# Optimization experiments

Measured on AMD Instinct MI355X. Metric: run time of the kernel, lower is better.

## Reference

```python
import jax, jax.numpy as jnp
import numpy as np

BSZ, L, D, K = 4, 4096, 512, 4


def setup_inputs() -> dict:
    key = jax.random.key(0)
    ks = jax.random.split(key, 8)
    n = jnp.arange(D, dtype=jnp.float32)
    f = jnp.sqrt(2.0 * n + 1.0)
    f = f / f.max()
    omega = jnp.exp(-f * np.float32(np.log(10000.0)))  # hippo_freqs(D)
    # freqs are strictly decreasing in n -> argsort descending == arange
    band_idx = jnp.argsort(-omega).reshape(K, D // K).astype(jnp.int32)
    B_vec = jnp.sqrt(2.0 * n + 1.0)
    B_vec = B_vec / B_vec.max()  # hippo_b_vector(D)
    return {
        "x": jax.random.normal(ks[0], (BSZ, L, D), dtype=jnp.float32),
        "z_prev": jax.random.normal(ks[1], (BSZ, L, D), dtype=jnp.float32),
        "W_psi": jax.random.normal(ks[2], (2 * D, D), dtype=jnp.float32) * 0.02,
        "b_psi": jnp.zeros((2 * D,), jnp.float32),
        "W_phi": jax.random.normal(ks[3], (2 * D, D), dtype=jnp.float32) * 0.02,
        "b_phi": jnp.zeros((2 * D,), jnp.float32),
        "W_gate": jax.random.normal(ks[4], (1, D), dtype=jnp.float32) * 0.02,
        "b_gate": jnp.zeros((1,), jnp.float32),
        "omega": omega,
        "log_gamma": jax.random.normal(ks[5], (D,), dtype=jnp.float32) - 3.0,
        "dt": jnp.array(0.1, jnp.float32),
        "surprise_gain": jnp.zeros((1,), jnp.float32),
        "tau": jnp.ones((1,), jnp.float32),
        "beta": jnp.zeros((1,), jnp.float32),
        "B_vec": B_vec,
        "band_idx": band_idx,
    }


def _exact_projection(z):
    # geodesic projection to zero-mean unit-std along last axis
    m = z.mean(-1, keepdims=True)
    v = ((z - m) ** 2).mean(-1, keepdims=True)
    return (z - m) / (jnp.sqrt(v) + 1e-6)


def reference(x, z_prev, W_psi, b_psi, W_phi, b_phi, W_gate, b_gate,
              omega, log_gamma, dt, surprise_gain, tau, beta, B_vec, band_idx):
    B_, L_, D_ = x.shape
    K_ = band_idx.shape[0]

    psi_raw = x @ W_psi.T + b_psi          # [B,L,2D]
    psi = jax.lax.complex(psi_raw[..., :D_], psi_raw[..., D_:])
    phi_raw = x @ W_phi.T + b_phi
    phi = jax.lax.complex(phi_raw[..., :D_], phi_raw[..., D_:])

    gate = jax.nn.sigmoid(x @ W_gate.T + b_gate)          # [B,L,1]
    surprise = jnp.abs(x - z_prev).mean(-1, keepdims=True)
    gate = gate * (1.0 + jnp.tanh(surprise_gain) * surprise)

    U = (gate * B_vec).astype(jnp.complex64) * psi        # [B,L,D] complex

    dta = jnp.abs(dt)
    lam = jax.lax.complex(-jnp.exp(log_gamma), omega)     # [D]
    t = jnp.arange(L_, dtype=jnp.float32)
    kernel = jnp.exp(lam[None, :] * (t[:, None] * dta))   # [L,D] complex, A^t

    n_fft = 2 * L_
    K_freq = jnp.fft.fft(kernel.T, n=n_fft, axis=1)                 # [D,2L]
    U_freq = jnp.fft.fft(jnp.transpose(U, (0, 2, 1)), n=n_fft, axis=2)  # [B,D,2L]
    H = jnp.fft.ifft(U_freq * K_freq[None], axis=2)[:, :, :L_]
    H = jnp.transpose(H, (0, 2, 1))                        # [B,L,D] complex

    H_proj = jax.lax.complex(_exact_projection(H.real), _exact_projection(H.imag))

    Hb = H_proj[:, :, band_idx]   # [B,L,K,band]
    Pb = phi[:, :, band_idx]
    alpha = (jnp.conj(Hb) * Pb).sum(-1, keepdims=True) / (D_ // K_)  # [B,L,K,1]
    c_k = jax.nn.softmax(jnp.abs(alpha) / jnp.clip(tau, 1e-4, None), axis=2)
    alpha_ig = alpha * c_k * K_
    density = (Hb.real ** 2 + Hb.imag ** 2).mean(-1, keepdims=True)
    alpha_fin = alpha_ig + (beta * density).astype(alpha_ig.dtype)
    out_bands = (Hb * alpha_fin).real                      # [B,L,K,band]

    out = jnp.zeros((B_, L_, D_), x.dtype).at[:, :, band_idx].set(out_bands)
    return out
```

## Files before the change

kernel.cpp:

```cpp
#include <hip/hip_runtime.h>
#include <hip/hip_bf16.h>
#include <math.h>

#define BSZ   4
#define LSEQ  4096
#define DDIM  512
#define KBAND 4
#define MROWS (BSZ*LSEQ)
#define BLD   (MROWS*DDIM)
#define CHUNK 16
#define NCH   (LSEQ/CHUNK)
#define NGRP  16
#define TBL   ((CHUNK+1)*DDIM)
#define NCOLS 2048

#define FRONT_CVT_BLOCKS  (MROWS/4)
#define FRONT_B_BLOCKS    ((NCOLS*64)/256)
#define FRONT_PREP_BLOCKS ((2*TBL+255)/256)

typedef __attribute__((ext_vector_type(8))) short  short8;
typedef __attribute__((ext_vector_type(8))) unsigned short u16x8;
typedef __attribute__((ext_vector_type(4))) unsigned short u16x4;
typedef __attribute__((ext_vector_type(4))) float  f32x4;

__device__ __forceinline__ unsigned short f2bf(float f) {
    unsigned int u = __float_as_uint(f);
    u = (u + 0x7FFFu + ((u >> 16) & 1u)) >> 16;
    return (unsigned short)u;
}
__device__ __forceinline__ float bf2f(unsigned short h) {
    return __uint_as_float(((unsigned int)h) << 16);
}

__device__ __forceinline__ void gld_lds16(const void* g, void* l) {
    __builtin_amdgcn_global_load_lds(
        (const __attribute__((address_space(1))) void*)g,
        (__attribute__((address_space(3))) void*)l, 16, 0, 0);
}

__global__ void k_front(const float* __restrict__ x,
                        const float* __restrict__ z_prev,
                        const float* __restrict__ Wg,
                        const float* __restrict__ bg,
                        const float* __restrict__ sg,
                        const float* __restrict__ Wpsi,
                        const float* __restrict__ Wphi,
                        const float* __restrict__ omega,
                        const float* __restrict__ log_gamma,
                        const float* __restrict__ dt,
                        const int*   __restrict__ band_idx,
                        float* __restrict__ gate,
                        unsigned short* __restrict__ Ahi,
                        unsigned short* __restrict__ Alo,
                        unsigned short* __restrict__ Bhi,
                        unsigned short* __restrict__ Blo,
                        float* __restrict__ apR, float* __restrict__ apI,
                        float* __restrict__ apgR, float* __restrict__ apgI,
                        int* __restrict__ bandOf, int* __restrict__ posOf)
{
    int bid = blockIdx.x;
    int tid = threadIdx.x;

    if (bid < FRONT_CVT_BLOCKS) {
        int m    = bid * 4 + (tid >> 6);
        int lane = tid & 63;
        const float4* xr = (const float4*)(x      + ((size_t)m << 9));
        const float4* zr = (const float4*)(z_prev + ((size_t)m << 9));
        const float4* wg = (const float4*)Wg;
        float dot = 0.f, sur = 0.f;
        int msw = m & 7;
#pragma unroll
        for (int i = 0; i < 2; i++) {
            int e = lane + i*64;
            float4 a = xr[e];
            float4 z = zr[e];
            float4 w = wg[e];
            dot += a.x*w.x + a.y*w.y + a.z*w.z + a.w*w.w;
            sur += fabsf(a.x-z.x) + fabsf(a.y-z.y) + fabsf(a.z-z.z) + fabsf(a.w-z.w);
            float fa[4] = {a.x, a.y, a.z, a.w};
            u16x4 h, l;
#pragma unroll
            for (int j = 0; j < 4; ++j) {
                unsigned short hb = f2bf(fa[j]);
                h[j] = hb;
                l[j] = f2bf(fa[j] - bf2f(hb));
            }
            int grp = e >> 1, half = e & 1;
            int chunk = grp >> 3, gs = grp & 7;
            int gd = gs ^ msw;
            size_t dst = ((size_t)m << 9) + chunk*64 + gd*8 + half*4;
            *(u16x4*)(Ahi + dst) = h;
            *(u16x4*)(Alo + dst) = l;
        }
#pragma unroll
        for (int mm = 32; mm; mm >>= 1) { dot += __shfl_xor(dot, mm); sur += __shfl_xor(sur, mm); }
        if (lane == 0) {
            float g = 1.f / (1.f + expf(-(dot + bg[0])));
            g *= (1.f + tanhf(sg[0]) * (sur * (1.f/512.f)));
            gate[m] = g;
        }
    } else if (bid < FRONT_CVT_BLOCKS + FRONT_B_BLOCKS) {
        int gid = (bid - FRONT_CVT_BLOCKS) * 256 + tid;
        int n = gid >> 6, grp = gid & 63;
        int chunk = grp >> 3, g = grp & 7;
        int se = chunk*64 + ((g ^ (n & 7)) << 3);
        const float* wp = (n < 1024) ? (Wpsi + ((size_t)n << 9) + se)
                                     : (Wphi + ((size_t)(n - 1024) << 9) + se);
        u16x8 h, l;
#pragma unroll
        for (int j = 0; j < 8; ++j) {
            float f = wp[j];
            unsigned short hb = f2bf(f);
            h[j] = hb;
            l[j] = f2bf(f - bf2f(hb));
        }
        size_t dst = ((size_t)n << 9) + grp*8;
        *(u16x8*)(Bhi + dst) = h;
        *(u16x8*)(Blo + dst) = l;
    } else {
        int gid = (bid - FRONT_CVT_BLOCKS - FRONT_B_BLOCKS) * 256 + tid;
        float dta = fabsf(dt[0]);
        if (gid < TBL) {
            int k = gid / DDIM, d = gid % DDIM;
            float g = -expf(log_gamma[d]);
            float w = omega[d];
            float e = expf(g * dta * (float)k);
            float s, c;
            sincosf(w * dta * (float)k, &s, &c);
            apR[gid] = e * c;
            apI[gid] = e * s;
        } else if (gid < 2*TBL) {
            int gg = gid - TBL;
            int k = gg / DDIM, d = gg % DDIM;
            float g = -expf(log_gamma[d]);
            float w = omega[d];
            float ph = dta * (float)(16 * k);
            float e = expf(g * ph);
            float s, c;
            sincosf(w * ph, &s, &c);
            apgR[gg] = e * c;
            apgI[gg] = e * s;
        }
        if (gid < DDIM) {
            int d = band_idx[gid];
            bandOf[d] = gid >> 7;
            posOf[d]  = gid & 127;
        }
    }
}

__global__ __launch_bounds__(256)
void k_gemm_bf16(const unsigned short* __restrict__ Ahi,
                 const unsigned short* __restrict__ Alo,
                 const unsigned short* __restrict__ Bhi,
                 const unsigned short* __restrict__ Blo,
                 const float* __restrict__ bpsi, const float* __restrict__ bphi,
                 float* __restrict__ psiR, float* __restrict__ psiI,
                 float* __restrict__ phiR, float* __restrict__ phiI)
{
    __shared__ __align__(16) char As[16384];
    __shared__ __align__(16) char Bs[16384];

    int bid = blockIdx.x;
    int wg  = (bid & 7) * 256 + (bid >> 3);
    int m0 = (wg >> 4) * 128;
    int n0 = (wg & 15) * 128;

    int tid  = threadIdx.x;
    int lane = tid & 63;
    int wv   = tid >> 6;
    int wm = wv >> 1, wn = wv & 1;
    int lr = lane & 15, lk = lane >> 4;

    f32x4 acc[4][4];
#pragma unroll
    for (int mi = 0; mi < 4; ++mi)
#pragma unroll
        for (int ni = 0; ni < 4; ++ni) acc[mi][ni] = (f32x4)0.f;

    for (int s = 0; s < 24; ++s) {
        const unsigned short* Asrc = (s >= 8 && s < 16) ? Alo : Ahi;
        const unsigned short* Bsrc = (s < 16) ? Bhi : Blo;
        int kb2 = (s & 7) << 7;

        __syncthreads();
#pragma unroll
        for (int i = 0; i < 4; ++i) {
            int flat = tid + i * 256;
            int r = flat >> 3, g = flat & 7;
            size_t goff = ((size_t)r << 10) + kb2 + g * 16;
            gld_lds16((const char*)Asrc + ((size_t)m0 << 10) + goff,
                      As + (wv * 64 + i * 256) * 16);
            gld_lds16((const char*)Bsrc + ((size_t)n0 << 10) + goff,
                      Bs + (wv * 64 + i * 256) * 16);
        }
        __syncthreads();

#pragma unroll
        for (int kk = 0; kk < 2; ++kk) {
            int tb = (kk * 64 + lk * 16) ^ ((lr & 7) << 4);
            short8 af[4], bfr[4];
#pragma unroll
            for (int mi = 0; mi < 4; ++mi) {
                int r = wm * 64 + mi * 16 + lr;
                af[mi] = *(const short8*)(As + r * 128 + tb);
            }
#pragma unroll
            for (int ni = 0; ni < 4; ++ni) {
                int r = wn * 64 + ni * 16 + lr;
                bfr[ni] = *(const short8*)(Bs + r * 128 + tb);
            }
#pragma unroll
            for (int mi = 0; mi < 4; ++mi)
#pragma unroll
                for (int ni = 0; ni < 4; ++ni)
                    acc[mi][ni] = __builtin_amdgcn_mfma_f32_16x16x32_bf16(
                        af[mi], bfr[ni], acc[mi][ni], 0, 0, 0);
        }
    }

#pragma unroll
    for (int ni = 0; ni < 4; ++ni) {
        int ncol = n0 + wn * 64 + ni * 16 + lr;
        float bias = (ncol < 1024) ? bpsi[ncol] : bphi[ncol - 1024];
        int p = ncol >> 9;
        float* plane = (p == 0) ? psiR : (p == 1) ? psiI : (p == 2) ? phiR : phiI;
        int col = ncol & 511;
#pragma unroll
        for (int mi = 0; mi < 4; ++mi) {
            int mrow = m0 + wm * 64 + mi * 16 + lk * 4;
#pragma unroll
            for (int j = 0; j < 4; ++j)
                plane[(size_t)(mrow + j) * 512 + col] = acc[mi][ni][j] + bias;
        }
    }
}

__launch_bounds__(512)
__global__ void k_scanc(const float* __restrict__ UR, const float* __restrict__ UI,
                        const float* __restrict__ gate,
                        const float* __restrict__ Bvec,
                        const float* __restrict__ apR, const float* __restrict__ apI,
                        float* __restrict__ carR, float* __restrict__ carI)
{
    int b = blockIdx.x >> 8;
    int c = blockIdx.x & 255;
    int d = threadIdx.x;
    float ar = apR[DDIM + d], ai = apI[DDIM + d];
    float bv = Bvec[d];
    int t0 = c * CHUNK;
    size_t base = ((size_t)b * LSEQ + t0) * DDIM + d;
    const float* grow = gate + (size_t)b * LSEQ + t0;

    float ur[CHUNK], ui[CHUNK];
#pragma unroll
    for (int t = 0; t < CHUNK; t++) {
        ur[t] = UR[base + (size_t)t * DDIM];
        ui[t] = UI[base + (size_t)t * DDIM];
    }
    float hr = 0.f, hi = 0.f;
#pragma unroll
    for (int t = 0; t < CHUNK; t++) {
        float g  = grow[t] * bv;
        float nr = ar*hr - ai*hi + g * ur[t];
        float ni = ar*hi + ai*hr + g * ui[t];
        hr = nr; hi = ni;
    }
    size_t ci = ((size_t)(b * NCH + c)) * DDIM + d;
    carR[ci] = hr; carI[ci] = hi;
}

__launch_bounds__(512)
__global__ void k_carry(float* __restrict__ carR, float* __restrict__ carI,
                        const float* __restrict__ apR, const float* __restrict__ apI,
                        const float* __restrict__ apgR, const float* __restrict__ apgI)
{
    __shared__ float totR[NGRP][32], totI[NGRP][32];
    __shared__ float excR[NGRP][32], excI[NGRP][32];

    int b    = blockIdx.x >> 4;
    int dblk = blockIdx.x & 15;
    int tid  = threadIdx.x;
    int cg   = tid >> 5;
    int dl   = tid & 31;
    int d    = dblk * 32 + dl;

    float qr = apR[CHUNK*DDIM + d], qi = apI[CHUNK*DDIM + d];
    size_t i0 = ((size_t)(b * NCH + cg * 16)) * DDIM + d;

    float pr[16], pi[16];
#pragma unroll
    for (int j = 0; j < 16; j++) {
        pr[j] = carR[i0 + (size_t)j * DDIM];
        pi[j] = carI[i0 + (size_t)j * DDIM];
    }
#pragma unroll
    for (int j = 1; j < 16; j++) {
        float nr = qr*pr[j-1] - qi*pi[j-1] + pr[j];
        float ni = qr*pi[j-1] + qi*pr[j-1] + pi[j];
        pr[j] = nr; pi[j] = ni;
    }
    totR[cg][dl] = pr[15];
    totI[cg][dl] = pi[15];
    __syncthreads();

    if (tid < 32) {
        int dd = dblk * 32 + tid;
        float Qr = apgR[16*DDIM + dd], Qi = apgI[16*DDIM + dd];
        float Pr = 0.f, Pi = 0.f;
#pragma unroll
        for (int g = 0; g < NGRP; g++) {
            excR[g][tid] = Pr; excI[g][tid] = Pi;
            float nr = Qr*Pr - Qi*Pi + totR[g][tid];
            float ni = Qr*Pi + Qi*Pr + totI[g][tid];
            Pr = nr; Pi = ni;
        }
    }
    __syncthreads();

    float Er = excR[cg][dl], Ei = excI[cg][dl];
    bool hasE = (cg > 0);
#pragma unroll
    for (int j = 0; j < 16; j++) {
        float rr = pr[j], ii = pi[j];
        if (hasE) {
            float fr = apgR[(j+1)*DDIM + d], fi = apgI[(j+1)*DDIM + d];
            rr += fr*Er - fi*Ei;
            ii += fr*Ei + fi*Er;
        }
        carR[i0 + (size_t)j * DDIM] = rr;
        carI[i0 + (size_t)j * DDIM] = ii;
    }
}

__launch_bounds__(512)
__global__ void k_out(const float* __restrict__ UR, const float* __restrict__ UI,
                      const float* __restrict__ phR, const float* __restrict__ phI,
                      const float* __restrict__ carR, const float* __restrict__ carI,
                      const float* __restrict__ apR, const float* __restrict__ apI,
                      const float* __restrict__ gate, const float* __restrict__ Bvec,
                      const float* __restrict__ tau, const float* __restrict__ beta,
                      float* __restrict__ out)
{
    __shared__ float p1[2][8][16];
    __shared__ float p2[2][8][16];

    int row0 = blockIdx.x * CHUNK;
    int b = row0 >> 12;
    int c = (row0 & 4095) >> 4;
    int d = threadIdx.x;
    int w = d >> 6, lane = d & 63;
    int kb = d >> 7;

    float ar = apR[DDIM + d], ai_ = apI[DDIM + d];
    float bv = Bvec[d];
    const float* grow = gate + row0;

    float cr = 0.f, cm = 0.f;
    bool hasCar = (c > 0);
    if (hasCar) {
        size_t ci = ((size_t)(b * NCH + (c - 1))) * DDIM + d;
        cr = carR[ci]; cm = carI[ci];
    }

    float tv = tau[0]; tv = (tv < 1e-4f) ? 1e-4f : tv;
    float bt_s = beta[0];

    float sr = 0.f, si_ = 0.f;

    for (int wnd = 0; wnd < 4; ++wnd) {
        int pb = wnd & 1;

        float hr[4], hi[4], ppr[4], ppi[4];
#pragma unroll
        for (int r = 0; r < 4; ++r) {
            int rowt = wnd*4 + r;
            size_t idx = ((size_t)(row0 + rowt) << 9) + d;
            ppr[r] = phR[idx]; ppi[r] = phI[idx];
            float g = grow[rowt] * bv;
            float nr = ar*sr - ai_*si_ + g * UR[idx];
            float ni = ar*si_ + ai_*sr + g * UI[idx];
            sr = nr; si_ = ni;
            hr[r] = sr; hi[r] = si_;
            if (hasCar) {
                float apr = apR[(rowt+1)*DDIM + d], api = apI[(rowt+1)*DDIM + d];
                hr[r] += apr*cr - api*cm;
                hi[r] += apr*cm + api*cr;
            }
        }

        float s0[4], s1[4], s2[4], s3[4];
#pragma unroll
        for (int r = 0; r < 4; ++r) {
            s0[r] = hr[r]; s1[r] = hi[r];
            s2[r] = hr[r]*hr[r]; s3[r] = hi[r]*hi[r];
        }
#pragma unroll
        for (int m = 32; m; m >>= 1) {
#pragma unroll
            for (int r = 0; r < 4; ++r) {
                s0[r] += __shfl_xor(s0[r], m); s1[r] += __shfl_xor(s1[r], m);
                s2[r] += __shfl_xor(s2[r], m); s3[r] += __shfl_xor(s3[r], m);
            }
        }
        if (lane == 0) {
#pragma unroll
            for (int r = 0; r < 4; ++r) {
                p1[pb][w][r*4+0] = s0[r]; p1[pb][w][r*4+1] = s1[r];
                p1[pb][w][r*4+2] = s2[r]; p1[pb][w][r*4+3] = s3[r];
            }
        }
        __syncthreads();

        float aR[4], aI[4], dn[4];
#pragma unroll
        for (int r = 0; r < 4; ++r) {
            float Sr = 0.f, Si = 0.f, Sr2 = 0.f, Si2 = 0.f;
#pragma unroll
            for (int ww = 0; ww < 8; ++ww) {
                Sr  += p1[pb][ww][r*4+0]; Si  += p1[pb][ww][r*4+1];
                Sr2 += p1[pb][ww][r*4+2]; Si2 += p1[pb][ww][r*4+3];
            }
            float mr = Sr * (1.f/512.f), mi = Si * (1.f/512.f);
            float vr = Sr2 * (1.f/512.f) - mr*mr;
            float vi = Si2 * (1.f/512.f) - mi*mi;
            float Hpr = (hr[r] - mr) / (sqrtf(vr) + 1e-6f);
            float Hpi = (hi[r] - mi) / (sqrtf(vi) + 1e-6f);
            hr[r] = Hpr; hi[r] = Hpi;
            aR[r] = Hpr*ppr[r] + Hpi*ppi[r];
            aI[r] = Hpr*ppi[r] - Hpi*ppr[r];
            dn[r] = Hpr*Hpr + Hpi*Hpi;
        }

#pragma unroll
        for (int m = 32; m; m >>= 1) {
#pragma unroll
            for (int r = 0; r < 4; ++r) {
                aR[r] += __shfl_xor(aR[r], m);
                aI[r] += __shfl_xor(aI[r], m);
                dn[r] += __shfl_xor(dn[r], m);
            }
        }
        if (lane == 0) {
#pragma unroll
            for (int r = 0; r < 4; ++r) {
                p2[pb][w][r*4+0] = aR[r]; p2[pb][w][r*4+1] = aI[r];
                p2[pb][w][r*4+2] = dn[r];
            }
        }
        __syncthreads();

#pragma unroll
        for (int r = 0; r < 4; ++r) {
            float aRk[4], aIk[4], dnk[4], mag[4];
            float mx = -1e30f;
#pragma unroll
            for (int k = 0; k < 4; k++) {
                aRk[k] = (p2[pb][2*k][r*4+0] + p2[pb][2*k+1][r*4+0]) * (1.f/128.f);
                aIk[k] = (p2[pb][2*k][r*4+1] + p2[pb][2*k+1][r*4+1]) * (1.f/128.f);
                dnk[k] = (p2[pb][2*k][r*4+2] + p2[pb][2*k+1][r*4+2]) * (1.f/128.f);
                mag[k] = sqrtf(aRk[k]*aRk[k] + aIk[k]*aIk[k]) / tv;
                mx = fmaxf(mx, mag[k]);
            }
            float se = 0.f, ek[4];
#pragma unroll
            for (int k = 0; k < 4; k++) { ek[k] = expf(mag[k] - mx); se += ek[k]; }
            float inv = 1.f / se;
            float ck  = ek[kb] * inv;
            float afR = aRk[kb] * ck * 4.f + bt_s * dnk[kb];
            float afI = aIk[kb] * ck * 4.f;
            size_t idx = ((size_t)(row0 + wnd*4 + r) << 9) + d;
            out[idx] = hr[r] * afR - hi[r] * afI;
        }
    }
}

extern "C" void kernel_launch(void* const* d_in, const int* in_sizes, int n_in,
                              void* d_out, int out_size, void* d_ws, size_t ws_size,
                              hipStream_t stream)
{
    const float* x        = (const float*)d_in[0];
    const float* z_prev   = (const float*)d_in[1];
    const float* W_psi    = (const float*)d_in[2];
    const float* b_psi    = (const float*)d_in[3];
    const float* W_phi    = (const float*)d_in[4];
    const float* b_phi    = (const float*)d_in[5];
    const float* W_gate   = (const float*)d_in[6];
    const float* b_gate   = (const float*)d_in[7];
    const float* omega    = (const float*)d_in[8];
    const float* log_gam  = (const float*)d_in[9];
    const float* dt       = (const float*)d_in[10];
    const float* sg       = (const float*)d_in[11];
    const float* tau      = (const float*)d_in[12];
    const float* beta     = (const float*)d_in[13];
    const float* B_vec    = (const float*)d_in[14];
    const int*   band_idx = (const int*)d_in[15];
    float* out = (float*)d_out;
    float* ws  = (float*)d_ws;

    float* psiR = ws;
    float* psiI = psiR + BLD;
    float* phiR = psiI + BLD;
    float* phiI = phiR + BLD;
    float* gate = phiI + BLD;
    float* apR  = gate + MROWS;
    float* apI  = apR + TBL;
    float* apgR = apI + TBL;
    float* apgI = apgR + TBL;
    float* carR = apgI + TBL;
    float* carI = carR + (size_t)BSZ*NCH*DDIM;
    int* bandOf = (int*)(carI + (size_t)BSZ*NCH*DDIM);
    int* posOf  = bandOf + DDIM;
    unsigned short* Bhi = (unsigned short*)(posOf + DDIM);
    unsigned short* Blo = Bhi + (size_t)NCOLS*512;

    unsigned short* Ahi = (unsigned short*)d_out;
    unsigned short* Alo = Ahi + (size_t)MROWS*512;

    k_front<<<FRONT_CVT_BLOCKS + FRONT_B_BLOCKS + FRONT_PREP_BLOCKS, 256, 0, stream>>>(
        x, z_prev, W_gate, b_gate, sg, W_psi, W_phi, omega, log_gam, dt, band_idx,
        gate, Ahi, Alo, Bhi, Blo, apR, apI, apgR, apgI, bandOf, posOf);

    k_gemm_bf16<<<(MROWS/128) * (NCOLS/128), 256, 0, stream>>>(
        Ahi, Alo, Bhi, Blo, b_psi, b_phi, psiR, psiI, phiR, phiI);

    k_scanc<<<BSZ * NCH, 512, 0, stream>>>(psiR, psiI, gate, B_vec, apR, apI, carR, carI);

    k_carry<<<BSZ * 16, 512, 0, stream>>>(carR, carI, apR, apI, apgR, apgI);

    k_out<<<MROWS/CHUNK, 512, 0, stream>>>(psiR, psiI, phiR, phiI, carR, carI,
                                           apR, apI, gate, B_vec, tau, beta, out);
}
```

Before: 407.1 us.

## Shrink scan chunk to four rows and vectorize scan/output kernels per thread

Reduces the chunked linear-recurrence chunk size from 16 to 4 timesteps and restructures the scan-carry and output kernels. Each thread now handles four contiguous channels with float4 loads, and each block handles four chunks. The carry kernel is rebalanced to 32 groups of 32 chunks. The output kernel drops its sequential four-window loop with double-buffered reductions in favour of a single pass with fewer syncs. The aim is more parallelism, wider memory accesses and a shorter serial dependency chain, at the cost of a larger carry array and a deeper carry-propagation pass.

```diff
diff --git a/kernel.cpp b/kernel.cpp
--- a/kernel.cpp
+++ b/kernel.cpp
@@ -5,18 +5,19 @@
 #define BSZ   4
 #define LSEQ  4096
 #define DDIM  512
-#define KBAND 4
 #define MROWS (BSZ*LSEQ)
 #define BLD   (MROWS*DDIM)
-#define CHUNK 16
+#define CHUNK 4
 #define NCH   (LSEQ/CHUNK)
-#define NGRP  16
-#define TBL   ((CHUNK+1)*DDIM)
+#define NCHG  (MROWS/CHUNK)
+#define NGRP  32
+#define TBLA  ((CHUNK+1)*DDIM)
+#define TBLG  (33*DDIM)
 #define NCOLS 2048
 
 #define FRONT_CVT_BLOCKS  (MROWS/4)
 #define FRONT_B_BLOCKS    ((NCOLS*64)/256)
-#define FRONT_PREP_BLOCKS ((2*TBL+255)/256)
+#define FRONT_PREP_BLOCKS ((TBLA+TBLG+255)/256)
 
 typedef __attribute__((ext_vector_type(8))) short  short8;
 typedef __attribute__((ext_vector_type(8))) unsigned short u16x8;
@@ -48,15 +49,13 @@
                         const float* __restrict__ omega,
                         const float* __restrict__ log_gamma,
                         const float* __restrict__ dt,
-                        const int*   __restrict__ band_idx,
                         float* __restrict__ gate,
                         unsigned short* __restrict__ Ahi,
                         unsigned short* __restrict__ Alo,
                         unsigned short* __restrict__ Bhi,
                         unsigned short* __restrict__ Blo,
                         float* __restrict__ apR, float* __restrict__ apI,
-                        float* __restrict__ apgR, float* __restrict__ apgI,
-                        int* __restrict__ bandOf, int* __restrict__ posOf)
+                        float* __restrict__ apgR, float* __restrict__ apgI)
 {
     int bid = blockIdx.x;
     int tid = threadIdx.x;
@@ -120,31 +119,27 @@
     } else {
         int gid = (bid - FRONT_CVT_BLOCKS - FRONT_B_BLOCKS) * 256 + tid;
         float dta = fabsf(dt[0]);
-        if (gid < TBL) {
+        if (gid < TBLA) {
             int k = gid / DDIM, d = gid % DDIM;
             float g = -expf(log_gamma[d]);
             float w = omega[d];
-            float e = expf(g * dta * (float)k);
+            float ph = dta * (float)k;
+            float e = expf(g * ph);
             float s, c;
-            sincosf(w * dta * (float)k, &s, &c);
+            sincosf(w * ph, &s, &c);
             apR[gid] = e * c;
             apI[gid] = e * s;
-        } else if (gid < 2*TBL) {
-            int gg = gid - TBL;
+        } else if (gid < TBLA + TBLG) {
+            int gg = gid - TBLA;
             int k = gg / DDIM, d = gg % DDIM;
             float g = -expf(log_gamma[d]);
             float w = omega[d];
-            float ph = dta * (float)(16 * k);
+            float ph = dta * (float)(4 * k);
             float e = expf(g * ph);
             float s, c;
             sincosf(w * ph, &s, &c);
             apgR[gg] = e * c;
             apgI[gg] = e * s;
-        }
-        if (gid < DDIM) {
-            int d = band_idx[gid];
-            bandOf[d] = gid >> 7;
-            posOf[d]  = gid & 127;
         }
     }
 }
@@ -243,31 +238,35 @@
                         const float* __restrict__ apR, const float* __restrict__ apI,
                         float* __restrict__ carR, float* __restrict__ carI)
 {
-    int b = blockIdx.x >> 8;
-    int c = blockIdx.x & 255;
-    int d = threadIdx.x;
-    float ar = apR[DDIM + d], ai = apI[DDIM + d];
-    float bv = Bvec[d];
-    int t0 = c * CHUNK;
-    size_t base = ((size_t)b * LSEQ + t0) * DDIM + d;
-    const float* grow = gate + (size_t)b * LSEQ + t0;
-
-    float ur[CHUNK], ui[CHUNK];
-#pragma unroll
-    for (int t = 0; t < CHUNK; t++) {
-        ur[t] = UR[base + (size_t)t * DDIM];
-        ui[t] = UI[base + (size_t)t * DDIM];
-    }
-    float hr = 0.f, hi = 0.f;
-#pragma unroll
-    for (int t = 0; t < CHUNK; t++) {
-        float g  = grow[t] * bv;
-        float nr = ar*hr - ai*hi + g * ur[t];
-        float ni = ar*hi + ai*hr + g * ui[t];
-        hr = nr; hi = ni;
-    }
-    size_t ci = ((size_t)(b * NCH + c)) * DDIM + d;
-    carR[ci] = hr; carI[ci] = hi;
+    int tid = threadIdx.x;
+    int g   = tid >> 7;
+    int t   = tid & 127;
+    int cc  = blockIdx.x * 4 + g;
+    int row0 = cc << 2;
+    int dbase = t << 2;
+
+    f32x4 ar = *(const f32x4*)(apR + DDIM + dbase);
+    f32x4 ai = *(const f32x4*)(apI + DDIM + dbase);
+    f32x4 bv = *(const f32x4*)(Bvec + dbase);
+
+    f32x4 sr = (f32x4)0.f, si = (f32x4)0.f;
+#pragma unroll
+    for (int r = 0; r < 4; ++r) {
+        size_t idx = ((size_t)(row0 + r) << 9) + dbase;
+        f32x4 uR = *(const f32x4*)(UR + idx);
+        f32x4 uI = *(const f32x4*)(UI + idx);
+        float gg = gate[row0 + r];
+#pragma unroll
+        for (int j = 0; j < 4; ++j) {
+            float gj = gg * bv[j];
+            float nr = ar[j]*sr[j] - ai[j]*si[j] + gj*uR[j];
+            float ni = ar[j]*si[j] + ai[j]*sr[j] + gj*uI[j];
+            sr[j] = nr; si[j] = ni;
+        }
+    }
+    size_t ci = ((size_t)cc << 9) + dbase;
+    *(f32x4*)(carR + ci) = sr;
+    *(f32x4*)(carI + ci) = si;
 }
 
 __launch_bounds__(512)
@@ -275,38 +274,38 @@
                         const float* __restrict__ apR, const float* __restrict__ apI,
                         const float* __restrict__ apgR, const float* __restrict__ apgI)
 {
-    __shared__ float totR[NGRP][32], totI[NGRP][32];
-    __shared__ float excR[NGRP][32], excI[NGRP][32];
-
-    int b    = blockIdx.x >> 4;
-    int dblk = blockIdx.x & 15;
+    __shared__ float totR[NGRP][16], totI[NGRP][16];
+    __shared__ float excR[NGRP][16], excI[NGRP][16];
+
+    int b    = blockIdx.x >> 5;
+    int dblk = blockIdx.x & 31;
     int tid  = threadIdx.x;
-    int cg   = tid >> 5;
-    int dl   = tid & 31;
-    int d    = dblk * 32 + dl;
+    int cg   = tid >> 4;
+    int dl   = tid & 15;
+    int d    = dblk * 16 + dl;
 
     float qr = apR[CHUNK*DDIM + d], qi = apI[CHUNK*DDIM + d];
-    size_t i0 = ((size_t)(b * NCH + cg * 16)) * DDIM + d;
-
-    float pr[16], pi[16];
-#pragma unroll
-    for (int j = 0; j < 16; j++) {
+    size_t i0 = ((size_t)(b * NCH + cg * 32)) * DDIM + d;
+
+    float pr[32], pi[32];
+#pragma unroll
+    for (int j = 0; j < 32; j++) {
         pr[j] = carR[i0 + (size_t)j * DDIM];
         pi[j] = carI[i0 + (size_t)j * DDIM];
     }
 #pragma unroll
-    for (int j = 1; j < 16; j++) {
+    for (int j = 1; j < 32; j++) {
         float nr = qr*pr[j-1] - qi*pi[j-1] + pr[j];
         float ni = qr*pi[j-1] + qi*pr[j-1] + pi[j];
         pr[j] = nr; pi[j] = ni;
     }
-    totR[cg][dl] = pr[15];
-    totI[cg][dl] = pi[15];
+    totR[cg][dl] = pr[31];
+    totI[cg][dl] = pi[31];
     __syncthreads();
 
-    if (tid < 32) {
-        int dd = dblk * 32 + tid;
-        float Qr = apgR[16*DDIM + dd], Qi = apgI[16*DDIM + dd];
+    if (tid < 16) {
+        int dd = dblk * 16 + tid;
+        float Qr = apgR[32*DDIM + dd], Qi = apgI[32*DDIM + dd];
         float Pr = 0.f, Pi = 0.f;
 #pragma unroll
         for (int g = 0; g < NGRP; g++) {
@@ -319,17 +318,11 @@
     __syncthreads();
 
     float Er = excR[cg][dl], Ei = excI[cg][dl];
-    bool hasE = (cg > 0);
-#pragma unroll
-    for (int j = 0; j < 16; j++) {
-        float rr = pr[j], ii = pi[j];
-        if (hasE) {
-            float fr = apgR[(j+1)*DDIM + d], fi = apgI[(j+1)*DDIM + d];
-            rr += fr*Er - fi*Ei;
-            ii += fr*Ei + fi*Er;
-        }
-        carR[i0 + (size_t)j * DDIM] = rr;
-        carI[i0 + (size_t)j * DDIM] = ii;
+#pragma unroll
+    for (int j = 0; j < 32; j++) {
+        float fr = apgR[(j+1)*DDIM + d], fi = apgI[(j+1)*DDIM + d];
+        carR[i0 + (size_t)j * DDIM] = pr[j] + fr*Er - fi*Ei;
+        carI[i0 + (size_t)j * DDIM] = pi[j] + fr*Ei + fi*Er;
     }
 }
 
@@ -342,136 +335,137 @@
                       const float* __restrict__ tau, const float* __restrict__ beta,
                       float* __restrict__ out)
 {
-    __shared__ float p1[2][8][16];
-    __shared__ float p2[2][8][16];
-
-    int row0 = blockIdx.x * CHUNK;
-    int b = row0 >> 12;
-    int c = (row0 & 4095) >> 4;
-    int d = threadIdx.x;
-    int w = d >> 6, lane = d & 63;
-    int kb = d >> 7;
-
-    float ar = apR[DDIM + d], ai_ = apI[DDIM + d];
-    float bv = Bvec[d];
-    const float* grow = gate + row0;
-
-    float cr = 0.f, cm = 0.f;
-    bool hasCar = (c > 0);
-    if (hasCar) {
-        size_t ci = ((size_t)(b * NCH + (c - 1))) * DDIM + d;
-        cr = carR[ci]; cm = carI[ci];
-    }
-
+    __shared__ float p1[4][2][16];
+    __shared__ float p2[4][4][12];
+
+    int tid  = threadIdx.x;
+    int g    = tid >> 7;
+    int t    = tid & 127;
+    int wv   = (tid >> 6) & 1;
+    int lane = tid & 63;
+    int cc   = blockIdx.x * 4 + g;
+    int ccb  = cc & (NCH - 1);
+    int row0 = cc << 2;
+    int dbase = t << 2;
+    int kb   = t >> 5;
+
+    f32x4 ar = *(const f32x4*)(apR + DDIM + dbase);
+    f32x4 ai = *(const f32x4*)(apI + DDIM + dbase);
+    f32x4 bv = *(const f32x4*)(Bvec + dbase);
+
+    f32x4 cr = (f32x4)0.f, cm = (f32x4)0.f;
+    if (ccb > 0) {
+        size_t ci = ((size_t)(cc - 1) << 9) + dbase;
+        cr = *(const f32x4*)(carR + ci);
+        cm = *(const f32x4*)(carI + ci);
+    }
     float tv = tau[0]; tv = (tv < 1e-4f) ? 1e-4f : tv;
     float bt_s = beta[0];
 
-    float sr = 0.f, si_ = 0.f;
-
-    for (int wnd = 0; wnd < 4; ++wnd) {
-        int pb = wnd & 1;
-
-        float hr[4], hi[4], ppr[4], ppi[4];
+    f32x4 hr[4], hi[4];
+    {
+        f32x4 sr = (f32x4)0.f, si = (f32x4)0.f;
 #pragma unroll
         for (int r = 0; r < 4; ++r) {
-            int rowt = wnd*4 + r;
-            size_t idx = ((size_t)(row0 + rowt) << 9) + d;
-            ppr[r] = phR[idx]; ppi[r] = phI[idx];
-            float g = grow[rowt] * bv;
-            float nr = ar*sr - ai_*si_ + g * UR[idx];
-            float ni = ar*si_ + ai_*sr + g * UI[idx];
-            sr = nr; si_ = ni;
-            hr[r] = sr; hi[r] = si_;
-            if (hasCar) {
-                float apr = apR[(rowt+1)*DDIM + d], api = apI[(rowt+1)*DDIM + d];
-                hr[r] += apr*cr - api*cm;
-                hi[r] += apr*cm + api*cr;
+            size_t idx = ((size_t)(row0 + r) << 9) + dbase;
+            f32x4 uR = *(const f32x4*)(UR + idx);
+            f32x4 uI = *(const f32x4*)(UI + idx);
+            float gg = gate[row0 + r];
+            f32x4 fr = *(const f32x4*)(apR + (r+1)*DDIM + dbase);
+            f32x4 fi = *(const f32x4*)(apI + (r+1)*DDIM + dbase);
+#pragma unroll
+            for (int j = 0; j < 4; ++j) {
+                float gj = gg * bv[j];
+                float nr = ar[j]*sr[j] - ai[j]*si[j] + gj*uR[j];
+                float ni = ar[j]*si[j] + ai[j]*sr[j] + gj*uI[j];
+                sr[j] = nr; si[j] = ni;
+                hr[r][j] = nr + fr[j]*cr[j] - fi[j]*cm[j];
+                hi[r][j] = ni + fr[j]*cm[j] + fi[j]*cr[j];
             }
         }
-
-        float s0[4], s1[4], s2[4], s3[4];
-#pragma unroll
-        for (int r = 0; r < 4; ++r) {
-            s0[r] = hr[r]; s1[r] = hi[r];
-            s2[r] = hr[r]*hr[r]; s3[r] = hi[r]*hi[r];
-        }
-#pragma unroll
-        for (int m = 32; m; m >>= 1) {
-#pragma unroll
-            for (int r = 0; r < 4; ++r) {
-                s0[r] += __shfl_xor(s0[r], m); s1[r] += __shfl_xor(s1[r], m);
-                s2[r] += __shfl_xor(s2[r], m); s3[r] += __shfl_xor(s3[r], m);
-            }
-        }
-        if (lane == 0) {
-#pragma unroll
-            for (int r = 0; r < 4; ++r) {
-                p1[pb][w][r*4+0] = s0[r]; p1[pb][w][r*4+1] = s1[r];
-                p1[pb][w][r*4+2] = s2[r]; p1[pb][w][r*4+3] = s3[r];
-            }
-        }
-        __syncthreads();
-
-        float aR[4], aI[4], dn[4];
-#pragma unroll
-        for (int r = 0; r < 4; ++r) {
-            float Sr = 0.f, Si = 0.f, Sr2 = 0.f, Si2 = 0.f;
-#pragma unroll
-            for (int ww = 0; ww < 8; ++ww) {
-                Sr  += p1[pb][ww][r*4+0]; Si  += p1[pb][ww][r*4+1];
-                Sr2 += p1[pb][ww][r*4+2]; Si2 += p1[pb][ww][r*4+3];
-            }
-            float mr = Sr * (1.f/512.f), mi = Si * (1.f/512.f);
-            float vr = Sr2 * (1.f/512.f) - mr*mr;
-            float vi = Si2 * (1.f/512.f) - mi*mi;
-            float Hpr = (hr[r] - mr) / (sqrtf(vr) + 1e-6f);
-            float Hpi = (hi[r] - mi) / (sqrtf(vi) + 1e-6f);
-            hr[r] = Hpr; hi[r] = Hpi;
-            aR[r] = Hpr*ppr[r] + Hpi*ppi[r];
-            aI[r] = Hpr*ppi[r] - Hpi*ppr[r];
-            dn[r] = Hpr*Hpr + Hpi*Hpi;
-        }
-
-#pragma unroll
-        for (int m = 32; m; m >>= 1) {
-#pragma unroll
-            for (int r = 0; r < 4; ++r) {
-                aR[r] += __shfl_xor(aR[r], m);
-                aI[r] += __shfl_xor(aI[r], m);
-                dn[r] += __shfl_xor(dn[r], m);
-            }
-        }
-        if (lane == 0) {
-#pragma unroll
-            for (int r = 0; r < 4; ++r) {
-                p2[pb][w][r*4+0] = aR[r]; p2[pb][w][r*4+1] = aI[r];
-                p2[pb][w][r*4+2] = dn[r];
-            }
-        }
-        __syncthreads();
-
-#pragma unroll
-        for (int r = 0; r < 4; ++r) {
-            float aRk[4], aIk[4], dnk[4], mag[4];
-            float mx = -1e30f;
-#pragma unroll
-            for (int k = 0; k < 4; k++) {
-                aRk[k] = (p2[pb][2*k][r*4+0] + p2[pb][2*k+1][r*4+0]) * (1.f/128.f);
-                aIk[k] = (p2[pb][2*k][r*4+1] + p2[pb][2*k+1][r*4+1]) * (1.f/128.f);
-                dnk[k] = (p2[pb][2*k][r*4+2] + p2[pb][2*k+1][r*4+2]) * (1.f/128.f);
-                mag[k] = sqrtf(aRk[k]*aRk[k] + aIk[k]*aIk[k]) / tv;
-                mx = fmaxf(mx, mag[k]);
-            }
-            float se = 0.f, ek[4];
-#pragma unroll
-            for (int k = 0; k < 4; k++) { ek[k] = expf(mag[k] - mx); se += ek[k]; }
-            float inv = 1.f / se;
-            float ck  = ek[kb] * inv;
-            float afR = aRk[kb] * ck * 4.f + bt_s * dnk[kb];
-            float afI = aIk[kb] * ck * 4.f;
-            size_t idx = ((size_t)(row0 + wnd*4 + r) << 9) + d;
-            out[idx] = hr[r] * afR - hi[r] * afI;
-        }
+    }
+
+    float s[16];
+#pragma unroll
+    for (int r = 0; r < 4; ++r) {
+        float a0=0.f, a1=0.f, a2=0.f, a3=0.f;
+#pragma unroll
+        for (int j = 0; j < 4; ++j) {
+            a0 += hr[r][j]; a1 += hi[r][j];
+            a2 += hr[r][j]*hr[r][j]; a3 += hi[r][j]*hi[r][j];
+        }
+        s[r*4+0]=a0; s[r*4+1]=a1; s[r*4+2]=a2; s[r*4+3]=a3;
+    }
+#pragma unroll
+    for (int m = 32; m; m >>= 1)
+#pragma unroll
+        for (int v = 0; v < 16; ++v) s[v] += __shfl_xor(s[v], m);
+    if (lane == 0)
+#pragma unroll
+        for (int v = 0; v < 16; ++v) p1[g][wv][v] = s[v];
+    __syncthreads();
+
+    float q[12];
+#pragma unroll
+    for (int r = 0; r < 4; ++r) {
+        float Sr  = p1[g][0][r*4+0] + p1[g][1][r*4+0];
+        float Si  = p1[g][0][r*4+1] + p1[g][1][r*4+1];
+        float Sr2 = p1[g][0][r*4+2] + p1[g][1][r*4+2];
+        float Si2 = p1[g][0][r*4+3] + p1[g][1][r*4+3];
+        float mr = Sr * (1.f/512.f), mi = Si * (1.f/512.f);
+        float vr = Sr2 * (1.f/512.f) - mr*mr;
+        float vi = Si2 * (1.f/512.f) - mi*mi;
+        float rvr = 1.f / (sqrtf(vr) + 1e-6f);
+        float rvi = 1.f / (sqrtf(vi) + 1e-6f);
+        size_t idx = ((size_t)(row0 + r) << 9) + dbase;
+        f32x4 pR = *(const f32x4*)(phR + idx);
+        f32x4 pI = *(const f32x4*)(phI + idx);
+        float aRs=0.f, aIs=0.f, dns=0.f;
+#pragma unroll
+        for (int j = 0; j < 4; ++j) {
+            float Hr = (hr[r][j] - mr) * rvr;
+            float Hi = (hi[r][j] - mi) * rvi;
+            hr[r][j] = Hr; hi[r][j] = Hi;
+            aRs += Hr*pR[j] + Hi*pI[j];
+            aIs += Hr*pI[j] - Hi*pR[j];
+            dns += Hr*Hr + Hi*Hi;
+        }
+        q[r*3+0]=aRs; q[r*3+1]=aIs; q[r*3+2]=dns;
+    }
+
+#pragma unroll
+    for (int m = 16; m; m >>= 1)
+#pragma unroll
+        for (int v = 0; v < 12; ++v) q[v] += __shfl_xor(q[v], m);
+    if ((lane & 31) == 0)
+#pragma unroll
+        for (int v = 0; v < 12; ++v) p2[g][kb][v] = q[v];
+    __syncthreads();
+
+#pragma unroll
+    for (int r = 0; r < 4; ++r) {
+        float aRk[4], aIk[4], dnk[4], mag[4];
+        float mx = -1e30f;
+#pragma unroll
+        for (int k = 0; k < 4; k++) {
+            aRk[k] = p2[g][k][r*3+0] * (1.f/128.f);
+            aIk[k] = p2[g][k][r*3+1] * (1.f/128.f);
+            dnk[k] = p2[g][k][r*3+2] * (1.f/128.f);
+            mag[k] = sqrtf(aRk[k]*aRk[k] + aIk[k]*aIk[k]) / tv;
+            mx = fmaxf(mx, mag[k]);
+        }
+        float se = 0.f, ek[4];
+#pragma unroll
+        for (int k = 0; k < 4; k++) { ek[k] = expf(mag[k] - mx); se += ek[k]; }
+        float inv = 1.f / se;
+        float ck  = ek[kb] * inv;
+        float afR = aRk[kb] * ck * 4.f + bt_s * dnk[kb];
+        float afI = aIk[kb] * ck * 4.f;
+        size_t idx = ((size_t)(row0 + r) << 9) + dbase;
+        f32x4 o;
+#pragma unroll
+        for (int j = 0; j < 4; ++j) o[j] = hr[r][j]*afR - hi[r][j]*afI;
+        *(f32x4*)(out + idx) = o;
     }
 }
 
@@ -494,7 +488,6 @@
     const float* tau      = (const float*)d_in[12];
     const float* beta     = (const float*)d_in[13];
     const float* B_vec    = (const float*)d_in[14];
-    const int*   band_idx = (const int*)d_in[15];
     float* out = (float*)d_out;
     float* ws  = (float*)d_ws;
 
@@ -504,30 +497,28 @@
     float* phiI = phiR + BLD;
     float* gate = phiI + BLD;
     float* apR  = gate + MROWS;
-    float* apI  = apR + TBL;
-    float* apgR = apI + TBL;
-    float* apgI = apgR + TBL;
-    float* carR = apgI + TBL;
-    float* carI = carR + (size_t)BSZ*NCH*DDIM;
-    int* bandOf = (int*)(carI + (size_t)BSZ*NCH*DDIM);
-    int* posOf  = bandOf + DDIM;
-    unsigned short* Bhi = (unsigned short*)(posOf + DDIM);
+    float* apI  = apR + TBLA;
+    float* apgR = apI + TBLA;
+    float* apgI = apgR + TBLG;
+    float* carR = apgI + TBLG;
+    float* carI = carR + (size_t)NCHG*DDIM;
+    unsigned short* Bhi = (unsigned short*)(carI + (size_t)NCHG*DDIM);
     unsigned short* Blo = Bhi + (size_t)NCOLS*512;
 
     unsigned short* Ahi = (unsigned short*)d_out;
     unsigned short* Alo = Ahi + (size_t)MROWS*512;
 
     k_front<<<FRONT_CVT_BLOCKS + FRONT_B_BLOCKS + FRONT_PREP_BLOCKS, 256, 0, stream>>>(
-        x, z_prev, W_gate, b_gate, sg, W_psi, W_phi, omega, log_gam, dt, band_idx,
-        gate, Ahi, Alo, Bhi, Blo, apR, apI, apgR, apgI, bandOf, posOf);
+        x, z_prev, W_gate, b_gate, sg, W_psi, W_phi, omega, log_gam, dt,
+        gate, Ahi, Alo, Bhi, Blo, apR, apI, apgR, apgI);
 
     k_gemm_bf16<<<(MROWS/128) * (NCOLS/128), 256, 0, stream>>>(
         Ahi, Alo, Bhi, Blo, b_psi, b_phi, psiR, psiI, phiR, phiI);
 
-    k_scanc<<<BSZ * NCH, 512, 0, stream>>>(psiR, psiI, gate, B_vec, apR, apI, carR, carI);
-
-    k_carry<<<BSZ * 16, 512, 0, stream>>>(carR, carI, apR, apI, apgR, apgI);
-
-    k_out<<<MROWS/CHUNK, 512, 0, stream>>>(psiR, psiI, phiR, phiI, carR, carI,
-                                           apR, apI, gate, B_vec, tau, beta, out);
-}
+    k_scanc<<<NCHG/4, 512, 0, stream>>>(psiR, psiI, gate, B_vec, apR, apI, carR, carI);
+
+    k_carry<<<BSZ * 32, 512, 0, stream>>>(carR, carI, apR, apI, apgR, apgI);
+
+    k_out<<<NCHG/4, 512, 0, stream>>>(psiR, psiI, phiR, phiI, carR, carI,
+                                      apR, apI, gate, B_vec, tau, beta, out);
+}
```

Measured after the change: 332.1 us. -18.4%, faster.
